# Optimization experiments

Hardware: AMD Instinct MI355X
Metric: run time of the kernel (lower is better)

The kernel has to match this reference:

```python
import jax, jax.numpy as jnp
import numpy as np

N_NODES = 100000
N_EDGES = 1600000
D = 128          # in_dim == out_dim
H = 8            # num_heads
DH = D // H      # head dim = 16
DFF = 2 * D
EPS_LN = 1e-5


def _ln(x, g, b):
    mu = jnp.mean(x, axis=-1, keepdims=True)
    var = jnp.var(x, axis=-1, keepdims=True)
    return (x - mu) * jax.lax.rsqrt(var + EPS_LN) * g + b


def setup_inputs() -> dict:
    key = jax.random.key(0)
    ks = jax.random.split(key, 12)
    s = 1.0 / np.sqrt(D)
    inp = {
        "h": jax.random.normal(ks[0], (N_NODES, D), jnp.float32),
        "src": jax.random.randint(ks[1], (N_EDGES,), 0, N_NODES, jnp.int32),
        "dst": jax.random.randint(ks[2], (N_EDGES,), 0, N_NODES, jnp.int32),
        "Wq": jax.random.normal(ks[3], (D, D), jnp.float32) * s,
        "Wk": jax.random.normal(ks[4], (D, D), jnp.float32) * s,
        "Wv": jax.random.normal(ks[5], (D, D), jnp.float32) * s,
        "Wo": jax.random.normal(ks[6], (D, D), jnp.float32) * s,
        "bo": jnp.zeros((D,), jnp.float32),
        "ln1_g": jnp.ones((D,), jnp.float32),
        "ln1_b": jnp.zeros((D,), jnp.float32),
        "W1": jax.random.normal(ks[7], (D, DFF), jnp.float32) * s,
        "b1": jnp.zeros((DFF,), jnp.float32),
        "W2": jax.random.normal(ks[8], (DFF, D), jnp.float32) * (1.0 / np.sqrt(DFF)),
        "b2": jnp.zeros((D,), jnp.float32),
        "ln2_g": jnp.ones((D,), jnp.float32),
        "ln2_b": jnp.zeros((D,), jnp.float32),
    }
    return inp


def reference(h, src, dst, Wq, Wk, Wv, Wo, bo, ln1_g, ln1_b, W1, b1, W2, b2, ln2_g, ln2_b):
    n = h.shape[0]
    # Q/K/V projections (no bias), split into heads: [N, H, DH]
    Q = (h @ Wq).reshape(n, H, DH)
    K = (h @ Wk).reshape(n, H, DH)
    V = (h @ Wv).reshape(n, H, DH)

    # edge-wise attention score: K[src] . Q[dst] / sqrt(DH), exp-clamped
    score = jnp.einsum("ehd,ehd->eh", K[src], Q[dst]) / np.sqrt(DH)  # [E, H]
    score = jnp.exp(jnp.clip(score, -5.0, 5.0))

    # weighted message sum + normalizer via segment reduce over dst
    m = V[src] * score[:, :, None]                                   # [E, H, DH]
    wV = jax.ops.segment_sum(m, dst, num_segments=n)                 # [N, H, DH]
    z = jax.ops.segment_sum(score, dst, num_segments=n)              # [N, H]

    h_attn = (wV / (z[:, :, None] + 1e-6)).reshape(n, D)

    # output projection + residual + LN
    x = h + (h_attn @ Wo + bo)
    x = _ln(x, ln1_g, ln1_b)

    # FFN + residual + LN
    y = jax.nn.relu(x @ W1 + b1) @ W2 + b2
    x = _ln(x + y, ln2_g, ln2_b)
    return x
```

## Files before the change

kernel.cpp:

```cpp
#include <hip/hip_runtime.h>
#include <hip/hip_bf16.h>
#include <math.h>


typedef __attribute__((ext_vector_type(8))) short bf16x8;
typedef __attribute__((ext_vector_type(4))) float f32x4;
typedef __attribute__((ext_vector_type(2))) _Float16 half2_t;

#define BSHIFT 9
#define BSIZE  512
#define KVROW  256

static __device__ __forceinline__ half2_t h2(unsigned u) {
    return __builtin_bit_cast(half2_t, u);
}

__global__ __launch_bounds__(256)
void qkv_fused(const float* __restrict__ h,
               const __hip_bfloat16* __restrict__ Wqt,
               const __hip_bfloat16* __restrict__ Wkt,
               const __hip_bfloat16* __restrict__ Wvt,
               unsigned short* __restrict__ Qh,
               unsigned char* __restrict__ KV,
               int N)
{
    __shared__ unsigned short As[64 * 136];
    __shared__ unsigned short Bs[128 * 136];

    const int tid  = threadIdx.x;
    const int row0 = blockIdx.x * 64;
    const int wave = tid >> 6, lane = tid & 63;
    const int quad = lane >> 4, l15 = lane & 15;

    #pragma unroll
    for (int it = 0; it < 4; ++it) {
        int i = tid + it * 256;
        int r = i >> 4, kb = i & 15;
        int rg = row0 + r; if (rg > N - 1) rg = N - 1;
        const float4 f0 = *(const float4*)&h[(size_t)rg * 128 + kb * 8];
        const float4 f1 = *(const float4*)&h[(size_t)rg * 128 + kb * 8 + 4];
        __hip_bfloat162 b01 = __float22bfloat162_rn(make_float2(f0.x, f0.y));
        __hip_bfloat162 b23 = __float22bfloat162_rn(make_float2(f0.z, f0.w));
        __hip_bfloat162 b45 = __float22bfloat162_rn(make_float2(f1.x, f1.y));
        __hip_bfloat162 b67 = __float22bfloat162_rn(make_float2(f1.z, f1.w));
        uint4 u;
        u.x = *(unsigned*)&b01; u.y = *(unsigned*)&b23;
        u.z = *(unsigned*)&b45; u.w = *(unsigned*)&b67;
        *(uint4*)&As[r * 136 + kb * 8] = u;
    }

    const __hip_bfloat16* Ws[3] = { Wqt, Wkt, Wvt };

    #pragma unroll
    for (int w = 0; w < 3; ++w) {
        #pragma unroll
        for (int it = 0; it < 8; ++it) {
            int i = tid + it * 256;
            int r = i >> 4, kb = i & 15;
            *(uint4*)&Bs[r * 136 + kb * 8] =
                *(const uint4*)&Ws[w][(size_t)r * 128 + kb * 8];
        }
        __syncthreads();

        f32x4 acc[8];
        #pragma unroll
        for (int t = 0; t < 8; ++t) acc[t] = (f32x4)0.f;

        const unsigned short* ap = &As[(wave * 16 + l15) * 136 + quad * 8];
        const unsigned short* bp = &Bs[l15 * 136 + quad * 8];
        #pragma unroll
        for (int ks = 0; ks < 4; ++ks) {
            bf16x8 a = *(const bf16x8*)(ap + ks * 32);
            #pragma unroll
            for (int t = 0; t < 8; ++t) {
                bf16x8 b = *(const bf16x8*)(bp + t * 16 * 136 + ks * 32);
                acc[t] = __builtin_amdgcn_mfma_f32_16x16x32_bf16(a, b, acc[t], 0, 0, 0);
            }
        }
        __syncthreads();

        const int rbase = row0 + wave * 16 + quad * 4;
        #pragma unroll
        for (int i = 0; i < 4; ++i) {
            int row = rbase + i;
            if (row >= N) continue;
            #pragma unroll
            for (int t = 0; t < 8; ++t) {
                float v = acc[t][i];
                if (w == 0) {
                    ((_Float16*)Qh)[(size_t)row * 128 + t * 16 + l15] = (_Float16)v;
                } else {
                    int pk = __builtin_amdgcn_cvt_pk_fp8_f32(v, 0.f, 0, false);
                    KV[(size_t)row * KVROW + (w == 1 ? 0 : 128) + t * 16 + l15] =
                        (unsigned char)(pk & 0xff);
                }
            }
        }
    }
}

template<int K, int YLOOP, bool RELU, bool LN, bool RESID, bool BIAS, bool RB16>
__global__ __launch_bounds__(256)
void gemm_mfma(const __hip_bfloat16* __restrict__ Ab, int lda,
               const __hip_bfloat16* __restrict__ Bt, int ldbt,
               const float* __restrict__ bias, const void* __restrict__ resid,
               const float* __restrict__ lng, const float* __restrict__ lnb,
               float* __restrict__ Cf, __hip_bfloat16* __restrict__ Cb, int ldc,
               int N)
{
    constexpr int CK = 128;
    static_assert(YLOOP == 1 || K == CK, "YLOOP>1 needs single K chunk");
    __shared__ unsigned short As[64 * 136];
    __shared__ unsigned short Bs[128 * 136];

    const int tid  = threadIdx.x;
    const int row0 = blockIdx.x * 64;
    const int wave = tid >> 6, lane = tid & 63;
    const int quad = lane >> 4, l15 = lane & 15;
    const int rbase = row0 + wave * 16 + quad * 4;

    for (int yy = 0; yy < YLOOP; ++yy) {
        const int col0 = yy * 128;

        f32x4 acc[8];
        #pragma unroll
        for (int t = 0; t < 8; ++t) acc[t] = (f32x4)0.f;

        for (int kc = 0; kc < K; kc += CK) {
            if (yy == 0) {
                #pragma unroll
                for (int it = 0; it < 4; ++it) {
                    int i = tid + it * 256;
                    int r = i >> 4, kb = i & 15;
                    int rg = row0 + r; if (rg > N - 1) rg = N - 1;
                    *(uint4*)&As[r * 136 + kb * 8] =
                        *(const uint4*)&Ab[(size_t)rg * lda + kc + kb * 8];
                }
            }
            #pragma unroll
            for (int it = 0; it < 8; ++it) {
                int i = tid + it * 256;
                int r = i >> 4, kb = i & 15;
                *(uint4*)&Bs[r * 136 + kb * 8] =
                    *(const uint4*)&Bt[(size_t)(col0 + r) * ldbt + kc + kb * 8];
            }
            __syncthreads();
            const unsigned short* ap = &As[(wave * 16 + l15) * 136 + quad * 8];
            const unsigned short* bp = &Bs[l15 * 136 + quad * 8];
            #pragma unroll
            for (int ks = 0; ks < 4; ++ks) {
                bf16x8 a = *(const bf16x8*)(ap + ks * 32);
                #pragma unroll
                for (int t = 0; t < 8; ++t) {
                    bf16x8 b = *(const bf16x8*)(bp + t * 16 * 136 + ks * 32);
                    acc[t] = __builtin_amdgcn_mfma_f32_16x16x32_bf16(a, b, acc[t], 0, 0, 0);
                }
            }
            __syncthreads();
        }

        float vals[8][4];
        #pragma unroll
        for (int t = 0; t < 8; ++t) {
            float bv = BIAS ? bias[col0 + t * 16 + l15] : 0.f;
            #pragma unroll
            for (int i = 0; i < 4; ++i) vals[t][i] = acc[t][i] + bv;
        }
        if (RESID) {
            #pragma unroll
            for (int i = 0; i < 4; ++i) {
                int row = rbase + i;
                if (row < N) {
                    if (RB16) {
                        const unsigned short* rb = (const unsigned short*)resid;
                        #pragma unroll
                        for (int t = 0; t < 8; ++t)
                            vals[t][i] += __uint_as_float(
                                (unsigned)rb[(size_t)row * 128 + t * 16 + l15] << 16);
                    } else {
                        const float* rf = (const float*)resid;
                        #pragma unroll
                        for (int t = 0; t < 8; ++t)
                            vals[t][i] += rf[(size_t)row * 128 + t * 16 + l15];
                    }
                }
            }
        }
        if (RELU) {
            #pragma unroll
            for (int t = 0; t < 8; ++t)
                #pragma unroll
                for (int i = 0; i < 4; ++i) vals[t][i] = fmaxf(vals[t][i], 0.f);
        }
        if (LN) {
            #pragma unroll
            for (int i = 0; i < 4; ++i) {
                float s = 0.f, sq = 0.f;
                #pragma unroll
                for (int t = 0; t < 8; ++t) { float v = vals[t][i]; s += v; sq += v * v; }
                s  += __shfl_xor(s, 1);  s  += __shfl_xor(s, 2);
                s  += __shfl_xor(s, 4);  s  += __shfl_xor(s, 8);
                sq += __shfl_xor(sq, 1); sq += __shfl_xor(sq, 2);
                sq += __shfl_xor(sq, 4); sq += __shfl_xor(sq, 8);
                float m  = s * (1.f / 128.f);
                float rs = rsqrtf(sq * (1.f / 128.f) - m * m + 1e-5f);
                #pragma unroll
                for (int t = 0; t < 8; ++t) {
                    float g = lng[t * 16 + l15], b = lnb[t * 16 + l15];
                    vals[t][i] = (vals[t][i] - m) * rs * g + b;
                }
            }
        }
        #pragma unroll
        for (int i = 0; i < 4; ++i) {
            int row = rbase + i;
            if (row >= N) continue;
            if (Cf) {
                #pragma unroll
                for (int t = 0; t < 8; ++t)
                    Cf[(size_t)row * ldc + col0 + t * 16 + l15] = vals[t][i];
            }
            if (Cb) {
                #pragma unroll
                for (int t = 0; t < 8; ++t)
                    Cb[(size_t)row * ldc + col0 + t * 16 + l15] =
                        __float2bfloat16(vals[t][i]);
            }
        }
    }
}

struct WArgs {
    const float* src[6];
    __hip_bfloat16* dst[6];
    int R[6], C[6];
};
__global__ __launch_bounds__(256)
void cast_w(WArgs wa, int* __restrict__ bCnt)
{
    if (blockIdx.x == 0 && blockIdx.y == 0) bCnt[threadIdx.x] = 0;
    int w = blockIdx.y;
    int R = wa.R[w], C = wa.C[w];
    int i = blockIdx.x * 256 + threadIdx.x;
    if (i >= R * C) return;
    int sh = (C == 256) ? 8 : 7;
    int r = i >> sh, c = i & (C - 1);
    wa.dst[w][(size_t)c * R + r] = __float2bfloat16(wa.src[w][i]);
}

__global__ __launch_bounds__(256)
void bucket_hist(const int* __restrict__ dst, int* __restrict__ bCnt,
                 int E, int chunk, int NB)
{
    __shared__ int bh[256];
    const int t = threadIdx.x;
    bh[t] = 0;
    __syncthreads();
    const int s0 = blockIdx.x * chunk;
    const int s1 = min(E, s0 + chunk);
    for (int i = s0 + t; i < s1; i += 256)
        atomicAdd(&bh[dst[i] >> BSHIFT], 1);
    __syncthreads();
    if (t < NB && bh[t]) atomicAdd(&bCnt[t], bh[t]);
}

__global__ __launch_bounds__(256)
void bucket_scan(const int* __restrict__ bCnt, int* __restrict__ bBase,
                 int* __restrict__ gCur, int* __restrict__ rowStart,
                 int N, int E, int NB)
{
    __shared__ int wsum[4];
    const int t = threadIdx.x, lane = t & 63, wv = t >> 6;
    int v = (t < NB) ? bCnt[t] : 0;
    const int s = v;
    for (int off = 1; off < 64; off <<= 1) {
        int u = __shfl_up(v, off);
        if (lane >= off) v += u;
    }
    if (lane == 63) wsum[wv] = v;
    __syncthreads();
    int add = 0;
    for (int w = 0; w < wv; ++w) add += wsum[w];
    const int excl = v + add - s;
    if (t <= NB) bBase[t] = excl;
    if (t < NB)  gCur[t]  = excl;
    if (t == 0)  rowStart[N] = E;
}

__global__ __launch_bounds__(256)
void partition_kernel(const int* __restrict__ src, const int* __restrict__ dst,
                      int* __restrict__ gCur, uint2* __restrict__ P,
                      int E, int chunk, int NB)
{
    __shared__ int ch[256];
    __shared__ int cur[256];
    const int t = threadIdx.x;
    ch[t] = 0;
    __syncthreads();
    const int s0 = blockIdx.x * chunk;
    const int s1 = min(E, s0 + chunk);
    for (int i = s0 + t; i < s1; i += 256)
        atomicAdd(&ch[dst[i] >> BSHIFT], 1);
    __syncthreads();
    if (t < NB) {
        int c = ch[t];
        cur[t] = c ? atomicAdd(&gCur[t], c) : 0;
    }
    __syncthreads();
    for (int i = s0 + t; i < s1; i += 256) {
        int d = dst[i];
        int pos = atomicAdd(&cur[d >> BSHIFT], 1);
        P[pos] = make_uint2((unsigned)src[i], (unsigned)d);
    }
}

__global__ __launch_bounds__(256)
void bucket_scatter(const uint2* __restrict__ P, const int* __restrict__ bBase,
                    int* __restrict__ rowStart, int* __restrict__ esrc, int N)
{
    __shared__ int hist[BSIZE];
    __shared__ int cur[BSIZE];
    __shared__ int wsum[4];

    const int b  = blockIdx.x;
    const int t  = threadIdx.x;
    const int d0 = b << BSHIFT;
    const int bb  = bBase[b];
    const int cnt = bBase[b + 1] - bb;

    hist[t] = 0; hist[t + 256] = 0;
    __syncthreads();
    for (int i = t; i < cnt; i += 256)
        atomicAdd(&hist[(int)P[bb + i].y - d0], 1);
    __syncthreads();

    {
        const int a0 = hist[2 * t], a1 = hist[2 * t + 1];
        int v = a0 + a1;
        const int s = v;
        const int lane = t & 63, wv = t >> 6;
        for (int off = 1; off < 64; off <<= 1) {
            int u = __shfl_up(v, off);
            if (lane >= off) v += u;
        }
        if (lane == 63) wsum[wv] = v;
        __syncthreads();
        int add = 0;
        for (int w = 0; w < wv; ++w) add += wsum[w];
        const int exclT = v + add - s;
        cur[2 * t]     = exclT;
        cur[2 * t + 1] = exclT + a0;
    }
    __syncthreads();
    for (int i = t; i < BSIZE; i += 256) {
        int d = d0 + i;
        if (d < N) rowStart[d] = bb + cur[i];
    }
    __syncthreads();
    for (int i = t; i < cnt; i += 256) {
        uint2 p = P[bb + i];
        int pos = atomicAdd(&cur[(int)p.y - d0], 1);
        esrc[bb + pos] = (int)p.x;
    }
}

__global__ __launch_bounds__(256)
void aggregate_kernel(unsigned short* __restrict__ Qp,
                      const unsigned char* __restrict__ KV,
                      const int* __restrict__ esrc,
                      const int* __restrict__ rowStart, int N)
{
    const int lane = threadIdx.x & 63;
    const int wid  = threadIdx.x >> 6;
    const int d    = blockIdx.x * 4 + wid;
    if (d >= N) return;

    const int c = lane & 15;
    const int g = lane >> 4;

    const uint4 qraw = *(const uint4*)(Qp + (size_t)d * 128u + c * 8);
    const half2_t q0 = h2(qraw.x), q1 = h2(qraw.y),
                  q2 = h2(qraw.z), q3 = h2(qraw.w);
    const float qf0 = (float)q0.x, qf1 = (float)q0.y;
    const float qf2 = (float)q1.x, qf3 = (float)q1.y;
    const float qf4 = (float)q2.x, qf5 = (float)q2.y;
    const float qf6 = (float)q3.x, qf7 = (float)q3.y;

    const int beg = rowStart[d];
    const int end = rowStart[d + 1];
    const int endm1 = end - 1;

    float a0 = 0.f, a1 = 0.f, a2 = 0.f, a3 = 0.f;
    float a4 = 0.f, a5 = 0.f, a6 = 0.f, a7 = 0.f, z = 0.f;
    const float S = 0.36067376022224085f;
    const float C = 7.2134752044448170f;

    const int nIt = (end - beg + 7) >> 3;
    #pragma unroll 2
    for (int it = 0; it < nIt; ++it) {
        const int ea = beg + it * 8 + g;
        const int eb = ea + 4;
        const bool va = ea < end;
        const bool vb = eb < end;
        const int sa = esrc[va ? ea : endm1];
        const int sb = esrc[vb ? eb : endm1];
        const unsigned char* pa = KV + (size_t)(unsigned)sa * (size_t)KVROW;
        const unsigned char* pb = KV + (size_t)(unsigned)sb * (size_t)KVROW;
        const uint2 ka = *(const uint2*)(pa + c * 8);
        const uint2 vA = *(const uint2*)(pa + 128 + c * 8);
        const uint2 kb = *(const uint2*)(pb + c * 8);
        const uint2 vB = *(const uint2*)(pb + 128 + c * 8);

        auto ka01 = __builtin_amdgcn_cvt_pk_f32_fp8(ka.x, false);
        auto ka23 = __builtin_amdgcn_cvt_pk_f32_fp8(ka.x, true);
        auto ka45 = __builtin_amdgcn_cvt_pk_f32_fp8(ka.y, false);
        auto ka67 = __builtin_amdgcn_cvt_pk_f32_fp8(ka.y, true);
        float p = ka01[0] * qf0 + ka01[1] * qf1 + ka23[0] * qf2 + ka23[1] * qf3
                + ka45[0] * qf4 + ka45[1] * qf5 + ka67[0] * qf6 + ka67[1] * qf7;
        p += __shfl_xor(p, 1);
        float se = exp2f(fminf(C, fmaxf(-C, p * S)));
        se = va ? se : 0.f;

        auto kb01 = __builtin_amdgcn_cvt_pk_f32_fp8(kb.x, false);
        auto kb23 = __builtin_amdgcn_cvt_pk_f32_fp8(kb.x, true);
        auto kb45 = __builtin_amdgcn_cvt_pk_f32_fp8(kb.y, false);
        auto kb67 = __builtin_amdgcn_cvt_pk_f32_fp8(kb.y, true);
        float p2 = kb01[0] * qf0 + kb01[1] * qf1 + kb23[0] * qf2 + kb23[1] * qf3
                 + kb45[0] * qf4 + kb45[1] * qf5 + kb67[0] * qf6 + kb67[1] * qf7;
        p2 += __shfl_xor(p2, 1);
        float se2 = exp2f(fminf(C, fmaxf(-C, p2 * S)));
        se2 = vb ? se2 : 0.f;

        auto va01 = __builtin_amdgcn_cvt_pk_f32_fp8(vA.x, false);
        auto va23 = __builtin_amdgcn_cvt_pk_f32_fp8(vA.x, true);
        auto va45 = __builtin_amdgcn_cvt_pk_f32_fp8(vA.y, false);
        auto va67 = __builtin_amdgcn_cvt_pk_f32_fp8(vA.y, true);
        a0 += va01[0] * se; a1 += va01[1] * se;
        a2 += va23[0] * se; a3 += va23[1] * se;
        a4 += va45[0] * se; a5 += va45[1] * se;
        a6 += va67[0] * se; a7 += va67[1] * se;
        z  += se;

        auto vb01 = __builtin_amdgcn_cvt_pk_f32_fp8(vB.x, false);
        auto vb23 = __builtin_amdgcn_cvt_pk_f32_fp8(vB.x, true);
        auto vb45 = __builtin_amdgcn_cvt_pk_f32_fp8(vB.y, false);
        auto vb67 = __builtin_amdgcn_cvt_pk_f32_fp8(vB.y, true);
        a0 += vb01[0] * se2; a1 += vb01[1] * se2;
        a2 += vb23[0] * se2; a3 += vb23[1] * se2;
        a4 += vb45[0] * se2; a5 += vb45[1] * se2;
        a6 += vb67[0] * se2; a7 += vb67[1] * se2;
        z  += se2;
    }

    a0 += __shfl_xor(a0, 16); a1 += __shfl_xor(a1, 16);
    a2 += __shfl_xor(a2, 16); a3 += __shfl_xor(a3, 16);
    a4 += __shfl_xor(a4, 16); a5 += __shfl_xor(a5, 16);
    a6 += __shfl_xor(a6, 16); a7 += __shfl_xor(a7, 16);
    z  += __shfl_xor(z, 16);
    a0 += __shfl_xor(a0, 32); a1 += __shfl_xor(a1, 32);
    a2 += __shfl_xor(a2, 32); a3 += __shfl_xor(a3, 32);
    a4 += __shfl_xor(a4, 32); a5 += __shfl_xor(a5, 32);
    a6 += __shfl_xor(a6, 32); a7 += __shfl_xor(a7, 32);
    z  += __shfl_xor(z, 32);

    if (g == 0) {
        const float inv = 1.0f / (z + 1e-6f);
        __hip_bfloat162 p0 = __float22bfloat162_rn(make_float2(a0 * inv, a1 * inv));
        __hip_bfloat162 p1 = __float22bfloat162_rn(make_float2(a2 * inv, a3 * inv));
        __hip_bfloat162 p2 = __float22bfloat162_rn(make_float2(a4 * inv, a5 * inv));
        __hip_bfloat162 p3 = __float22bfloat162_rn(make_float2(a6 * inv, a7 * inv));
        uint4 o;
        o.x = *(unsigned*)&p0; o.y = *(unsigned*)&p1;
        o.z = *(unsigned*)&p2; o.w = *(unsigned*)&p3;
        *(uint4*)(Qp + (size_t)d * 128u + c * 8) = o;
    }
}

extern "C" void kernel_launch(void* const* d_in, const int* in_sizes, int n_in,
                              void* d_out, int out_size, void* d_ws, size_t ws_size,
                              hipStream_t stream)
{
    const float* h    = (const float*)d_in[0];
    const int*   src  = (const int*)  d_in[1];
    const int*   dst  = (const int*)  d_in[2];
    const float* Wq   = (const float*)d_in[3];
    const float* Wk   = (const float*)d_in[4];
    const float* Wv   = (const float*)d_in[5];
    const float* Wo   = (const float*)d_in[6];
    const float* bo   = (const float*)d_in[7];
    const float* ln1g = (const float*)d_in[8];
    const float* ln1b = (const float*)d_in[9];
    const float* W1   = (const float*)d_in[10];
    const float* b1   = (const float*)d_in[11];
    const float* W2   = (const float*)d_in[12];
    const float* b2   = (const float*)d_in[13];
    const float* ln2g = (const float*)d_in[14];
    const float* ln2b = (const float*)d_in[15];

    const int N = in_sizes[0] / 128;
    const int E = in_sizes[1];
    const int NB = (N + BSIZE - 1) >> BSHIFT;

    unsigned short* Qh = (unsigned short*)d_ws;
    unsigned char*  KVc = (unsigned char*)(Qh + (size_t)N * 128);
    __hip_bfloat16* Xh = (__hip_bfloat16*)(KVc + (size_t)N * KVROW);
    __hip_bfloat16* Wt = (__hip_bfloat16*)(Xh + (size_t)N * 128);
    __hip_bfloat16* Wqt = Wt;
    __hip_bfloat16* Wkt = Wqt + 16384;
    __hip_bfloat16* Wvt = Wkt + 16384;
    __hip_bfloat16* Wot = Wvt + 16384;
    __hip_bfloat16* W1t = Wot + 16384;
    __hip_bfloat16* W2t = W1t + 32768;
    int* ib       = (int*)(W2t + 32768);
    int* bCnt     = ib;
    int* bBase    = ib + 256;
    int* gCur     = ib + 514;
    int* rowStart = ib + 770;
    int* esrc     = ib + 770 + N + 2;
    uint2* P      = (uint2*)Xh;
    __hip_bfloat16* Th = (__hip_bfloat16*)Qh;

    const dim3 blk(256);
    const int  nb    = (N + 63) / 64;
    const int  chunk = (E + 255) / 256;

    WArgs wa;
    wa.src[0] = Wq; wa.src[1] = Wk; wa.src[2] = Wv; wa.src[3] = Wo; wa.src[4] = W1; wa.src[5] = W2;
    wa.dst[0] = Wqt; wa.dst[1] = Wkt; wa.dst[2] = Wvt; wa.dst[3] = Wot; wa.dst[4] = W1t; wa.dst[5] = W2t;
    wa.R[0] = wa.R[1] = wa.R[2] = wa.R[3] = 128; wa.R[4] = 128; wa.R[5] = 256;
    wa.C[0] = wa.C[1] = wa.C[2] = wa.C[3] = 128; wa.C[4] = 256; wa.C[5] = 128;
    cast_w<<<dim3(128, 6), blk, 0, stream>>>(wa, bCnt);

    qkv_fused<<<dim3(nb), blk, 0, stream>>>(h, Wqt, Wkt, Wvt, Qh, KVc, N);

    bucket_hist<<<dim3(256), blk, 0, stream>>>(dst, bCnt, E, chunk, NB);
    bucket_scan<<<dim3(1), blk, 0, stream>>>(bCnt, bBase, gCur, rowStart, N, E, NB);
    partition_kernel<<<dim3(256), blk, 0, stream>>>(src, dst, gCur, P, E, chunk, NB);
    bucket_scatter<<<dim3(NB), blk, 0, stream>>>(P, bBase, rowStart, esrc, N);

    aggregate_kernel<<<dim3((N + 3) / 4), blk, 0, stream>>>(Qh, KVc, esrc, rowStart, N);

    gemm_mfma<128,1,false,true,true,true,false><<<dim3(nb), blk, 0, stream>>>(
        (const __hip_bfloat16*)Qh, 128, Wot, 128, bo, h, ln1g, ln1b,
        nullptr, Xh, 128, N);

    gemm_mfma<128,2,true,false,false,true,false><<<dim3(nb), blk, 0, stream>>>(
        Xh, 128, W1t, 128, b1, nullptr, nullptr, nullptr,
        nullptr, Th, 256, N);

    gemm_mfma<256,1,false,true,true,true,true><<<dim3(nb), blk, 0, stream>>>(
        Th, 256, W2t, 256, b2, Xh, ln2g, ln2b,
        (float*)d_out, nullptr, 128, N);
}
```

Measured before the change: 359.8 us.

## Fuse output projection, LN1 and FFN first layer; merge bucket scan into histogram

Adds a kernel that runs the Wo projection, bias, residual and LayerNorm, keeps the normalized rows in shared memory, and then runs the W1+ReLU GEMM on them. The separate W1 GEMM no longer has to re-read Xh from global memory. Th moves to its own workspace region because Qh is still being read in the same kernel. The bucket scan launch is folded into bucket_hist with a last-block-done counter, which removes one tiny launch at the cost of an atomic and a threadfence per block.

Result: slower. 372.6 us (+3.6%).

```diff
diff --git a/kernel.cpp b/kernel.cpp
--- a/kernel.cpp
+++ b/kernel.cpp
@@ -94,6 +94,148 @@
                     KV[(size_t)row * KVROW + (w == 1 ? 0 : 128) + t * 16 + l15] =
                         (unsigned char)(pk & 0xff);
                 }
+            }
+        }
+    }
+}
+
+__global__ __launch_bounds__(256)
+void ln1_w1(const __hip_bfloat16* __restrict__ Ah,
+            const __hip_bfloat16* __restrict__ Wot,
+            const __hip_bfloat16* __restrict__ W1t,
+            const float* __restrict__ bo,
+            const float* __restrict__ hres,
+            const float* __restrict__ ln1g, const float* __restrict__ ln1b,
+            const float* __restrict__ b1,
+            __hip_bfloat16* __restrict__ Xh,
+            __hip_bfloat16* __restrict__ Th, int N)
+{
+    __shared__ unsigned short As[64 * 136];
+    __shared__ unsigned short Bs[128 * 136];
+
+    const int tid  = threadIdx.x;
+    const int row0 = blockIdx.x * 64;
+    const int wave = tid >> 6, lane = tid & 63;
+    const int quad = lane >> 4, l15 = lane & 15;
+    const int rbase = row0 + wave * 16 + quad * 4;
+
+    #pragma unroll
+    for (int it = 0; it < 4; ++it) {
+        int i = tid + it * 256;
+        int r = i >> 4, kb = i & 15;
+        int rg = row0 + r; if (rg > N - 1) rg = N - 1;
+        *(uint4*)&As[r * 136 + kb * 8] =
+            *(const uint4*)&Ah[(size_t)rg * 128 + kb * 8];
+    }
+    #pragma unroll
+    for (int it = 0; it < 8; ++it) {
+        int i = tid + it * 256;
+        int r = i >> 4, kb = i & 15;
+        *(uint4*)&Bs[r * 136 + kb * 8] =
+            *(const uint4*)&Wot[(size_t)r * 128 + kb * 8];
+    }
+    __syncthreads();
+
+    f32x4 acc[8];
+    #pragma unroll
+    for (int t = 0; t < 8; ++t) acc[t] = (f32x4)0.f;
+    {
+        const unsigned short* ap = &As[(wave * 16 + l15) * 136 + quad * 8];
+        const unsigned short* bp = &Bs[l15 * 136 + quad * 8];
+        #pragma unroll
+        for (int ks = 0; ks < 4; ++ks) {
+            bf16x8 a = *(const bf16x8*)(ap + ks * 32);
+            #pragma unroll
+            for (int t = 0; t < 8; ++t) {
+                bf16x8 b = *(const bf16x8*)(bp + t * 16 * 136 + ks * 32);
+                acc[t] = __builtin_amdgcn_mfma_f32_16x16x32_bf16(a, b, acc[t], 0, 0, 0);
+            }
+        }
+    }
+
+    float vals[8][4];
+    #pragma unroll
+    for (int t = 0; t < 8; ++t) {
+        float bv = bo[t * 16 + l15];
+        #pragma unroll
+        for (int i = 0; i < 4; ++i) vals[t][i] = acc[t][i] + bv;
+    }
+    #pragma unroll
+    for (int i = 0; i < 4; ++i) {
+        int row = rbase + i;
+        if (row < N) {
+            #pragma unroll
+            for (int t = 0; t < 8; ++t)
+                vals[t][i] += hres[(size_t)row * 128 + t * 16 + l15];
+        }
+    }
+    #pragma unroll
+    for (int i = 0; i < 4; ++i) {
+        float s = 0.f, sq = 0.f;
+        #pragma unroll
+        for (int t = 0; t < 8; ++t) { float v = vals[t][i]; s += v; sq += v * v; }
+        s  += __shfl_xor(s, 1);  s  += __shfl_xor(s, 2);
+        s  += __shfl_xor(s, 4);  s  += __shfl_xor(s, 8);
+        sq += __shfl_xor(sq, 1); sq += __shfl_xor(sq, 2);
+        sq += __shfl_xor(sq, 4); sq += __shfl_xor(sq, 8);
+        float m  = s * (1.f / 128.f);
+        float rs = rsqrtf(sq * (1.f / 128.f) - m * m + 1e-5f);
+        #pragma unroll
+        for (int t = 0; t < 8; ++t) {
+            float g = ln1g[t * 16 + l15], b = ln1b[t * 16 + l15];
+            vals[t][i] = (vals[t][i] - m) * rs * g + b;
+        }
+    }
+    #pragma unroll
+    for (int i = 0; i < 4; ++i) {
+        int row = rbase + i;
+        int rl  = wave * 16 + quad * 4 + i;
+        #pragma unroll
+        for (int t = 0; t < 8; ++t) {
+            __hip_bfloat16 xb = __float2bfloat16(vals[t][i]);
+            As[rl * 136 + t * 16 + l15] = *(unsigned short*)&xb;
+            if (row < N)
+                Xh[(size_t)row * 128 + t * 16 + l15] = xb;
+        }
+    }
+
+    #pragma unroll
+    for (int half = 0; half < 2; ++half) {
+        __syncthreads();
+        #pragma unroll
+        for (int it = 0; it < 8; ++it) {
+            int i = tid + it * 256;
+            int r = i >> 4, kb = i & 15;
+            *(uint4*)&Bs[r * 136 + kb * 8] =
+                *(const uint4*)&W1t[(size_t)(half * 128 + r) * 128 + kb * 8];
+        }
+        __syncthreads();
+
+        f32x4 a1[8];
+        #pragma unroll
+        for (int t = 0; t < 8; ++t) a1[t] = (f32x4)0.f;
+        {
+            const unsigned short* ap = &As[(wave * 16 + l15) * 136 + quad * 8];
+            const unsigned short* bp = &Bs[l15 * 136 + quad * 8];
+            #pragma unroll
+            for (int ks = 0; ks < 4; ++ks) {
+                bf16x8 a = *(const bf16x8*)(ap + ks * 32);
+                #pragma unroll
+                for (int t = 0; t < 8; ++t) {
+                    bf16x8 b = *(const bf16x8*)(bp + t * 16 * 136 + ks * 32);
+                    a1[t] = __builtin_amdgcn_mfma_f32_16x16x32_bf16(a, b, a1[t], 0, 0, 0);
+                }
+            }
+        }
+        #pragma unroll
+        for (int i = 0; i < 4; ++i) {
+            int row = rbase + i;
+            if (row >= N) continue;
+            #pragma unroll
+            for (int t = 0; t < 8; ++t) {
+                float v = fmaxf(a1[t][i] + b1[half * 128 + t * 16 + l15], 0.f);
+                Th[(size_t)row * 256 + half * 128 + t * 16 + l15] =
+                    __float2bfloat16(v);
             }
         }
     }
@@ -236,9 +378,12 @@
     int R[6], C[6];
 };
 __global__ __launch_bounds__(256)
-void cast_w(WArgs wa, int* __restrict__ bCnt)
-{
-    if (blockIdx.x == 0 && blockIdx.y == 0) bCnt[threadIdx.x] = 0;
+void cast_w(WArgs wa, int* __restrict__ bCnt, int* __restrict__ done)
+{
+    if (blockIdx.x == 0 && blockIdx.y == 0) {
+        bCnt[threadIdx.x] = 0;
+        if (threadIdx.x == 0) *done = 0;
+    }
     int w = blockIdx.y;
     int R = wa.R[w], C = wa.C[w];
     int i = blockIdx.x * 256 + threadIdx.x;
@@ -250,9 +395,13 @@
 
 __global__ __launch_bounds__(256)
 void bucket_hist(const int* __restrict__ dst, int* __restrict__ bCnt,
-                 int E, int chunk, int NB)
+                 int* __restrict__ bBase, int* __restrict__ gCur,
+                 int* __restrict__ rowStart, int* __restrict__ done,
+                 int N, int E, int chunk, int NB)
 {
     __shared__ int bh[256];
+    __shared__ int lastFlag;
+    __shared__ int wsum[4];
     const int t = threadIdx.x;
     bh[t] = 0;
     __syncthreads();
@@ -262,17 +411,15 @@
         atomicAdd(&bh[dst[i] >> BSHIFT], 1);
     __syncthreads();
     if (t < NB && bh[t]) atomicAdd(&bCnt[t], bh[t]);
-}
-
-__global__ __launch_bounds__(256)
-void bucket_scan(const int* __restrict__ bCnt, int* __restrict__ bBase,
-                 int* __restrict__ gCur, int* __restrict__ rowStart,
-                 int N, int E, int NB)
-{
-    __shared__ int wsum[4];
-    const int t = threadIdx.x, lane = t & 63, wv = t >> 6;
-    int v = (t < NB) ? bCnt[t] : 0;
-    const int s = v;
+
+    __threadfence();
+    if (t == 0) lastFlag = (atomicAdd(done, 1) == (int)gridDim.x - 1) ? 1 : 0;
+    __syncthreads();
+    if (!lastFlag) return;
+
+    const int lane = t & 63, wv = t >> 6;
+    int v = (t < NB) ? atomicAdd(&bCnt[t], 0) : 0;
+    const int sv = v;
     for (int off = 1; off < 64; off <<= 1) {
         int u = __shfl_up(v, off);
         if (lane >= off) v += u;
@@ -281,7 +428,7 @@
     __syncthreads();
     int add = 0;
     for (int w = 0; w < wv; ++w) add += wsum[w];
-    const int excl = v + add - s;
+    const int excl = v + add - sv;
     if (t <= NB) bBase[t] = excl;
     if (t < NB)  gCur[t]  = excl;
     if (t == 0)  rowStart[N] = E;
@@ -504,7 +651,8 @@
     unsigned short* Qh = (unsigned short*)d_ws;
     unsigned char*  KVc = (unsigned char*)(Qh + (size_t)N * 128);
     __hip_bfloat16* Xh = (__hip_bfloat16*)(KVc + (size_t)N * KVROW);
-    __hip_bfloat16* Wt = (__hip_bfloat16*)(Xh + (size_t)N * 128);
+    __hip_bfloat16* Th = (__hip_bfloat16*)(Xh + (size_t)N * 128);
+    __hip_bfloat16* Wt = (__hip_bfloat16*)(Th + (size_t)N * 256);
     __hip_bfloat16* Wqt = Wt;
     __hip_bfloat16* Wkt = Wqt + 16384;
     __hip_bfloat16* Wvt = Wkt + 16384;
@@ -514,11 +662,11 @@
     int* ib       = (int*)(W2t + 32768);
     int* bCnt     = ib;
     int* bBase    = ib + 256;
+    int* done     = ib + 513;
     int* gCur     = ib + 514;
     int* rowStart = ib + 770;
     int* esrc     = ib + 770 + N + 2;
     uint2* P      = (uint2*)Xh;
-    __hip_bfloat16* Th = (__hip_bfloat16*)Qh;
 
     const dim3 blk(256);
     const int  nb    = (N + 63) / 64;
@@ -529,24 +677,19 @@
     wa.dst[0] = Wqt; wa.dst[1] = Wkt; wa.dst[2] = Wvt; wa.dst[3] = Wot; wa.dst[4] = W1t; wa.dst[5] = W2t;
     wa.R[0] = wa.R[1] = wa.R[2] = wa.R[3] = 128; wa.R[4] = 128; wa.R[5] = 256;
     wa.C[0] = wa.C[1] = wa.C[2] = wa.C[3] = 128; wa.C[4] = 256; wa.C[5] = 128;
-    cast_w<<<dim3(128, 6), blk, 0, stream>>>(wa, bCnt);
+    cast_w<<<dim3(128, 6), blk, 0, stream>>>(wa, bCnt, done);
 
     qkv_fused<<<dim3(nb), blk, 0, stream>>>(h, Wqt, Wkt, Wvt, Qh, KVc, N);
 
-    bucket_hist<<<dim3(256), blk, 0, stream>>>(dst, bCnt, E, chunk, NB);
-    bucket_scan<<<dim3(1), blk, 0, stream>>>(bCnt, bBase, gCur, rowStart, N, E, NB);
+    bucket_hist<<<dim3(256), blk, 0, stream>>>(dst, bCnt, bBase, gCur,
+                                               rowStart, done, N, E, chunk, NB);
     partition_kernel<<<dim3(256), blk, 0, stream>>>(src, dst, gCur, P, E, chunk, NB);
     bucket_scatter<<<dim3(NB), blk, 0, stream>>>(P, bBase, rowStart, esrc, N);
 
     aggregate_kernel<<<dim3((N + 3) / 4), blk, 0, stream>>>(Qh, KVc, esrc, rowStart, N);
 
-    gemm_mfma<128,1,false,true,true,true,false><<<dim3(nb), blk, 0, stream>>>(
-        (const __hip_bfloat16*)Qh, 128, Wot, 128, bo, h, ln1g, ln1b,
-        nullptr, Xh, 128, N);
-
-    gemm_mfma<128,2,true,false,false,true,false><<<dim3(nb), blk, 0, stream>>>(
-        Xh, 128, W1t, 128, b1, nullptr, nullptr, nullptr,
-        nullptr, Th, 256, N);
+    ln1_w1<<<dim3(nb), blk, 0, stream>>>(
+        (const __hip_bfloat16*)Qh, Wot, W1t, bo, h, ln1g, ln1b, b1, Xh, Th, N);
 
     gemm_mfma<256,1,false,true,true,true,true><<<dim3(nb), blk, 0, stream>>>(
         Th, 256, W2t, 256, b2, Xh, ln2g, ln2b,
```
